# Kernel tuning notes

Measured on AMD Instinct MI355X. Metric: run time of the kernel, lower is better.

## Reference

```python
import jax, jax.numpy as jnp
import numpy as np

B, C, W, H = 16, 256, 64, 64
D = C // 8  # query/key head dim = 32


def setup_inputs() -> dict:
    key = jax.random.key(0)
    k1, k2, k3 = jax.random.split(key, 3)
    x = jax.random.normal(k1, (B, C, W, H), dtype=jnp.float32)
    # 1x1 conv weights, squeezed to [out_ch, in_ch]
    Wq = jax.random.normal(k2, (D, C), dtype=jnp.float32) * (1.0 / np.sqrt(C))
    Wk = jax.random.normal(k3, (D, C), dtype=jnp.float32) * (1.0 / np.sqrt(C))
    return {"x": x, "Wq": Wq, "Wk": Wk}


def reference(x, Wq, Wk):
    # x: [B, C, W, H]. Attention is row-restricted: independent per (b, w),
    # attending over the H axis. (value_conv in the torch module is unused.)
    q = jnp.einsum('bcwh,dc->bwhd', x, Wq)          # [B, W, H, D]
    k = jnp.einsum('bcwh,dc->bwdh', x, Wk)          # [B, W, D, H]
    energy = jnp.einsum('bwhd,bwdj->bwhj', q, k)    # [B, W, H, H] (unscaled)
    attn = jax.nn.softmax(energy, axis=-1)          # softmax over keys j
    v = jnp.transpose(x, (0, 2, 1, 3))              # [B, W, C, H]
    # torch: bmm(v, attn^T): out[c, i] = sum_j v[c, j] * attn[i, j]
    out = jnp.einsum('bwcj,bwij->bwci', v, attn)    # [B, W, C, H]
    out = jnp.transpose(out, (0, 2, 1, 3))          # [B, C, W, H]
    return out * x                                  # elementwise gate
```

## Files before the change

kernel.cpp:

```cpp
#include <hip/hip_runtime.h>

#define BB 16
#define CCH 256
#define WWD 64
#define HHT 64
#define WH (WWD*HHT)

typedef short bf16x8 __attribute__((ext_vector_type(8)));
typedef float f32x4  __attribute__((ext_vector_type(4)));

__device__ __forceinline__ short f2bf(float f) {
  unsigned u = __builtin_bit_cast(unsigned, f);
  u += 0x7fffu + ((u >> 16) & 1u);
  return (short)(u >> 16);
}
__device__ __forceinline__ float bf2f(short s) {
  unsigned u = ((unsigned)(unsigned short)s) << 16;
  return __builtin_bit_cast(float, u);
}

__global__ __launch_bounds__(256) void selfattn_kernel(
    const float* __restrict__ x, const float* __restrict__ Wq,
    const float* __restrict__ Wk, float* __restrict__ out) {
  __shared__ float    q_lds[64 * 36];
  __shared__ float    k_lds[32 * 64];
  __shared__ unsigned attnT[64 * 64];

  const int tid  = threadIdx.x;
  const int lane = tid & 63;
  const int wave = tid >> 6;
  const int blk  = blockIdx.x;
  const int b    = blk >> 6;
  const int w    = blk & 63;

  const float* xb = x   + (size_t)b * CCH * WH + (size_t)w * HHT;
  float*       ob = out + (size_t)b * CCH * WH + (size_t)w * HHT;

  const int d0 = __builtin_amdgcn_readfirstlane(wave * 8);
  float qa[8] = {0,0,0,0,0,0,0,0};
  float ka[8] = {0,0,0,0,0,0,0,0};
  for (int cb = 0; cb < CCH; cb += 32) {
    float xv[32];
    #pragma unroll
    for (int cc = 0; cc < 32; ++cc) xv[cc] = xb[(size_t)(cb + cc) * WH + lane];
    #pragma unroll
    for (int dd = 0; dd < 8; ++dd) {
      const float4* wq4 = (const float4*)(Wq + (size_t)(d0 + dd) * CCH + cb);
      const float4* wk4 = (const float4*)(Wk + (size_t)(d0 + dd) * CCH + cb);
      float qacc = qa[dd], kacc = ka[dd];
      #pragma unroll
      for (int c4 = 0; c4 < 8; ++c4) {
        const float4 wq = wq4[c4];
        const float4 wk = wk4[c4];
        qacc += xv[4*c4+0]*wq.x + xv[4*c4+1]*wq.y + xv[4*c4+2]*wq.z + xv[4*c4+3]*wq.w;
        kacc += xv[4*c4+0]*wk.x + xv[4*c4+1]*wk.y + xv[4*c4+2]*wk.z + xv[4*c4+3]*wk.w;
      }
      qa[dd] = qacc; ka[dd] = kacc;
    }
  }
  #pragma unroll
  for (int dd = 0; dd < 8; ++dd) {
    q_lds[lane*36 + d0 + dd] = qa[dd];
    k_lds[(d0+dd)*64 + lane] = ka[dd];
  }
  __syncthreads();

  float kc[32];
  #pragma unroll
  for (int d = 0; d < 32; ++d) kc[d] = k_lds[d*64 + lane];

  const int h0 = __builtin_amdgcn_readfirstlane(wave * 16);
  for (int hh = 0; hh < 16; ++hh) {
    const int h = h0 + hh;
    const float4* qrow = (const float4*)&q_lds[h*36];
    float e = 0.f;
    #pragma unroll
    for (int d4 = 0; d4 < 8; ++d4) {
      const float4 qv = qrow[d4];
      e += qv.x*kc[4*d4+0] + qv.y*kc[4*d4+1] + qv.z*kc[4*d4+2] + qv.w*kc[4*d4+3];
    }
    float m = e;
    #pragma unroll
    for (int off = 32; off >= 1; off >>= 1) m = fmaxf(m, __shfl_xor(m, off, 64));
    const float ex = __expf(e - m);
    float s = ex;
    #pragma unroll
    for (int off = 32; off >= 1; off >>= 1) s += __shfl_xor(s, off, 64);
    const float p  = ex / s;
    const short ph = f2bf(p);
    const short pl = f2bf(p - bf2f(ph));
    attnT[lane*64 + (h ^ (lane & 31))] =
        (unsigned)(unsigned short)ph | ((unsigned)(unsigned short)pl << 16);
  }
  __syncthreads();

  const int g   = lane >> 4;
  const int r16 = lane & 15;

  bf16x8 bh[4][2], bl[4][2];
  #pragma unroll
  for (int it = 0; it < 4; ++it) {
    const int i = it*16 + r16;
    #pragma unroll
    for (int ks = 0; ks < 2; ++ks) {
      bf16x8 hfr, lfr;
      #pragma unroll
      for (int t = 0; t < 8; ++t) {
        const int j = ks*32 + g*8 + t;
        const unsigned pw = attnT[j*64 + (i ^ (j & 31))];
        hfr[t] = (short)(pw & 0xffffu);
        lfr[t] = (short)(pw >> 16);
      }
      bh[it][ks] = hfr; bl[it][ks] = lfr;
    }
  }

  const int c0w = __builtin_amdgcn_readfirstlane(wave * 64);
  #pragma unroll
  for (int ct = 0; ct < 4; ++ct) {
    const int crow = c0w + ct*16 + r16;
    bf16x8 xh[2], xl[2];
    #pragma unroll
    for (int ks = 0; ks < 2; ++ks) {
      const float4 f0 = *(const float4*)(xb + (size_t)crow*WH + ks*32 + g*8);
      const float4 f1 = *(const float4*)(xb + (size_t)crow*WH + ks*32 + g*8 + 4);
      const float xs[8] = {f0.x,f0.y,f0.z,f0.w,f1.x,f1.y,f1.z,f1.w};
      bf16x8 hfr, lfr;
      #pragma unroll
      for (int t = 0; t < 8; ++t) {
        hfr[t] = f2bf(xs[t]);
        lfr[t] = f2bf(xs[t] - bf2f(hfr[t]));
      }
      xh[ks] = hfr; xl[ks] = lfr;
    }
    #pragma unroll
    for (int it = 0; it < 4; ++it) {
      f32x4 acc = {0.f, 0.f, 0.f, 0.f};
      #pragma unroll
      for (int ks = 0; ks < 2; ++ks) {
        acc = __builtin_amdgcn_mfma_f32_16x16x32_bf16(xh[ks], bh[it][ks], acc, 0, 0, 0);
        acc = __builtin_amdgcn_mfma_f32_16x16x32_bf16(xh[ks], bl[it][ks], acc, 0, 0, 0);
        acc = __builtin_amdgcn_mfma_f32_16x16x32_bf16(xl[ks], bh[it][ks], acc, 0, 0, 0);
      }
      const int i = it*16 + r16;
      #pragma unroll
      for (int r = 0; r < 4; ++r) {
        const int c = c0w + ct*16 + g*4 + r;
        const float xg = xb[(size_t)c*WH + i];
        ob[(size_t)c*WH + i] = acc[r] * xg;
      }
    }
  }
}

extern "C" void kernel_launch(void* const* d_in, const int* in_sizes, int n_in,
                              void* d_out, int out_size, void* d_ws, size_t ws_size,
                              hipStream_t stream) {
  (void)in_sizes; (void)n_in; (void)d_ws; (void)ws_size; (void)out_size;
  const float* x  = (const float*)d_in[0];
  const float* Wq = (const float*)d_in[1];
  const float* Wk = (const float*)d_in[2];
  float* out = (float*)d_out;
  dim3 grid(BB * WWD);
  dim3 block(256);
  hipLaunchKernelGGL(selfattn_kernel, grid, block, 0, stream, x, Wq, Wk, out);
}
```

Before: 189.3 us.

## Compute Q/K projection with split-bf16 MFMA using pre-split weights in workspace

```diff
diff --git a/kernel.cpp b/kernel.cpp
--- a/kernel.cpp
+++ b/kernel.cpp
@@ -19,7 +19,173 @@
   return __builtin_bit_cast(float, u);
 }
 
-__global__ __launch_bounds__(256) void selfattn_kernel(
+__global__ __launch_bounds__(256) void wsplit_kernel(
+    const float* __restrict__ Wq, const float* __restrict__ Wk,
+    short* __restrict__ ws) {
+  const int gid    = blockIdx.x * 256 + threadIdx.x;
+  const int fragid = gid >> 6;
+  const int lane   = gid & 63;
+  const int dp = (fragid >> 3) * 16 + (lane & 15);
+  const int cb = (fragid & 7) * 32 + ((lane >> 4) & 3) * 8;
+  const float* Wrow = (dp < 32) ? (Wq + (size_t)dp * CCH)
+                                : (Wk + (size_t)(dp - 32) * CCH);
+  bf16x8 hfr, lfr;
+  #pragma unroll
+  for (int t = 0; t < 8; ++t) {
+    const float v = Wrow[cb + t];
+    const short h = f2bf(v);
+    hfr[t] = h;
+    lfr[t] = f2bf(v - bf2f(h));
+  }
+  *(bf16x8*)(ws + (size_t)gid * 8)         = hfr;
+  *(bf16x8*)(ws + 16384 + (size_t)gid * 8) = lfr;
+}
+
+__global__ __launch_bounds__(256, 4) void selfattn_kernel(
+    const float* __restrict__ x, const short* __restrict__ ws,
+    float* __restrict__ out) {
+  __shared__ float    q_lds[64 * 36];
+  __shared__ float    k_lds[32 * 64];
+  __shared__ unsigned attnT[64 * 64];
+
+  const int tid  = threadIdx.x;
+  const int lane = tid & 63;
+  const int wave = tid >> 6;
+  const int g    = lane >> 4;
+  const int r16  = lane & 15;
+  const int blk  = blockIdx.x;
+  const int b    = blk >> 6;
+  const int w    = blk & 63;
+
+  const float* xb = x   + (size_t)b * CCH * WH + (size_t)w * HHT;
+  float*       ob = out + (size_t)b * CCH * WH + (size_t)w * HHT;
+
+  {
+    const int nt = wave;
+    bf16x8 xbh[8], xbl[8];
+    #pragma unroll
+    for (int kt = 0; kt < 8; ++kt) {
+      bf16x8 hfr, lfr;
+      #pragma unroll
+      for (int t = 0; t < 8; ++t) {
+        const int c = kt*32 + g*8 + t;
+        const float v = xb[(size_t)c * WH + nt*16 + r16];
+        const short h = f2bf(v);
+        hfr[t] = h;
+        lfr[t] = f2bf(v - bf2f(h));
+      }
+      xbh[kt] = hfr; xbl[kt] = lfr;
+    }
+    const short* wsh = ws;
+    const short* wsl = ws + 16384;
+    #pragma unroll
+    for (int mt = 0; mt < 4; ++mt) {
+      f32x4 acc = {0.f, 0.f, 0.f, 0.f};
+      #pragma unroll
+      for (int kt = 0; kt < 8; ++kt) {
+        const bf16x8 ah = *(const bf16x8*)(wsh + (size_t)((mt*8 + kt)*64 + lane) * 8);
+        const bf16x8 al = *(const bf16x8*)(wsl + (size_t)((mt*8 + kt)*64 + lane) * 8);
+        acc = __builtin_amdgcn_mfma_f32_16x16x32_bf16(ah, xbh[kt], acc, 0, 0, 0);
+        acc = __builtin_amdgcn_mfma_f32_16x16x32_bf16(ah, xbl[kt], acc, 0, 0, 0);
+        acc = __builtin_amdgcn_mfma_f32_16x16x32_bf16(al, xbh[kt], acc, 0, 0, 0);
+      }
+      #pragma unroll
+      for (int r = 0; r < 4; ++r) {
+        const int dp = mt*16 + g*4 + r;
+        const int h  = nt*16 + r16;
+        if (mt < 2) q_lds[h*36 + dp] = acc[r];
+        else        k_lds[(dp - 32)*64 + h] = acc[r];
+      }
+    }
+  }
+  __syncthreads();
+
+  float kc[32];
+  #pragma unroll
+  for (int d = 0; d < 32; ++d) kc[d] = k_lds[d*64 + lane];
+
+  const int h0 = __builtin_amdgcn_readfirstlane(wave * 16);
+  for (int hh = 0; hh < 16; ++hh) {
+    const int h = h0 + hh;
+    const float4* qrow = (const float4*)&q_lds[h*36];
+    float e = 0.f;
+    #pragma unroll
+    for (int d4 = 0; d4 < 8; ++d4) {
+      const float4 qv = qrow[d4];
+      e += qv.x*kc[4*d4+0] + qv.y*kc[4*d4+1] + qv.z*kc[4*d4+2] + qv.w*kc[4*d4+3];
+    }
+    float m = e;
+    #pragma unroll
+    for (int off = 32; off >= 1; off >>= 1) m = fmaxf(m, __shfl_xor(m, off, 64));
+    const float ex = __expf(e - m);
+    float s = ex;
+    #pragma unroll
+    for (int off = 32; off >= 1; off >>= 1) s += __shfl_xor(s, off, 64);
+    const float p  = ex / s;
+    const short ph = f2bf(p);
+    const short pl = f2bf(p - bf2f(ph));
+    attnT[lane*64 + (h ^ (lane & 31))] =
+        (unsigned)(unsigned short)ph | ((unsigned)(unsigned short)pl << 16);
+  }
+  __syncthreads();
+
+  bf16x8 bh[4][2], bl[4][2];
+  #pragma unroll
+  for (int it = 0; it < 4; ++it) {
+    const int i = it*16 + r16;
+    #pragma unroll
+    for (int ks = 0; ks < 2; ++ks) {
+      bf16x8 hfr, lfr;
+      #pragma unroll
+      for (int t = 0; t < 8; ++t) {
+        const int j = ks*32 + g*8 + t;
+        const unsigned pw = attnT[j*64 + (i ^ (j & 31))];
+        hfr[t] = (short)(pw & 0xffffu);
+        lfr[t] = (short)(pw >> 16);
+      }
+      bh[it][ks] = hfr; bl[it][ks] = lfr;
+    }
+  }
+
+  const int c0w = __builtin_amdgcn_readfirstlane(wave * 64);
+  #pragma unroll
+  for (int ct = 0; ct < 4; ++ct) {
+    const int crow = c0w + ct*16 + r16;
+    bf16x8 xh[2], xl[2];
+    #pragma unroll
+    for (int ks = 0; ks < 2; ++ks) {
+      const float4 f0 = *(const float4*)(xb + (size_t)crow*WH + ks*32 + g*8);
+      const float4 f1 = *(const float4*)(xb + (size_t)crow*WH + ks*32 + g*8 + 4);
+      const float xs[8] = {f0.x,f0.y,f0.z,f0.w,f1.x,f1.y,f1.z,f1.w};
+      bf16x8 hfr, lfr;
+      #pragma unroll
+      for (int t = 0; t < 8; ++t) {
+        hfr[t] = f2bf(xs[t]);
+        lfr[t] = f2bf(xs[t] - bf2f(hfr[t]));
+      }
+      xh[ks] = hfr; xl[ks] = lfr;
+    }
+    #pragma unroll
+    for (int it = 0; it < 4; ++it) {
+      f32x4 acc = {0.f, 0.f, 0.f, 0.f};
+      #pragma unroll
+      for (int ks = 0; ks < 2; ++ks) {
+        acc = __builtin_amdgcn_mfma_f32_16x16x32_bf16(xh[ks], bh[it][ks], acc, 0, 0, 0);
+        acc = __builtin_amdgcn_mfma_f32_16x16x32_bf16(xh[ks], bl[it][ks], acc, 0, 0, 0);
+        acc = __builtin_amdgcn_mfma_f32_16x16x32_bf16(xl[ks], bh[it][ks], acc, 0, 0, 0);
+      }
+      const int i = it*16 + r16;
+      #pragma unroll
+      for (int r = 0; r < 4; ++r) {
+        const int c = c0w + ct*16 + g*4 + r;
+        const float xg = xb[(size_t)c*WH + i];
+        ob[(size_t)c*WH + i] = acc[r] * xg;
+      }
+    }
+  }
+}
+
+__global__ __launch_bounds__(256) void selfattn_fb(
     const float* __restrict__ x, const float* __restrict__ Wq,
     const float* __restrict__ Wk, float* __restrict__ out) {
   __shared__ float    q_lds[64 * 36];
@@ -96,7 +262,6 @@
 
   const int g   = lane >> 4;
   const int r16 = lane & 15;
-
   bf16x8 bh[4][2], bl[4][2];
   #pragma unroll
   for (int it = 0; it < 4; ++it) {
@@ -156,12 +321,18 @@
 extern "C" void kernel_launch(void* const* d_in, const int* in_sizes, int n_in,
                               void* d_out, int out_size, void* d_ws, size_t ws_size,
                               hipStream_t stream) {
-  (void)in_sizes; (void)n_in; (void)d_ws; (void)ws_size; (void)out_size;
+  (void)in_sizes; (void)n_in; (void)out_size;
   const float* x  = (const float*)d_in[0];
   const float* Wq = (const float*)d_in[1];
   const float* Wk = (const float*)d_in[2];
   float* out = (float*)d_out;
-  dim3 grid(BB * WWD);
-  dim3 block(256);
-  hipLaunchKernelGGL(selfattn_kernel, grid, block, 0, stream, x, Wq, Wk, out);
-}
+  if (ws_size >= 65536) {
+    hipLaunchKernelGGL(wsplit_kernel, dim3(8), dim3(256), 0, stream,
+                       Wq, Wk, (short*)d_ws);
+    hipLaunchKernelGGL(selfattn_kernel, dim3(BB * WWD), dim3(256), 0, stream,
+                       x, (const short*)d_ws, out);
+  } else {
+    hipLaunchKernelGGL(selfattn_fb, dim3(BB * WWD), dim3(256), 0, stream,
+                       x, Wq, Wk, out);
+  }
+}
```

After: 153.4 us. 19.0% less time.
